# Kernel tuning notes

Hardware: AMD Instinct MI355X
Metric: run time of the kernel (lower is better)

Reference implementation:

```python
import jax, jax.numpy as jnp
import numpy as np

N = 50000      # nodes
E = 800000     # edges
D = 256        # embed_dim
H = 8          # num_heads
HD = D // H    # head_dim = 32
F = 4 * D      # feedforward_dim = 1024
SCALE = D ** -0.5  # note: module scales by embed_dim**-0.5, not head_dim
EPS = 1e-5


def setup_inputs() -> dict:
    key = jax.random.key(0)
    ks = jax.random.split(key, 10)
    x = jax.random.normal(ks[0], (N, D), dtype=jnp.float32)
    edge_indices = jax.random.randint(ks[1], (2, E), 0, N, dtype=jnp.int32)
    s = 0.02
    return {
        "x": x,
        "edge_indices": edge_indices,
        "w_qkv": jax.random.normal(ks[2], (D, 3 * D), dtype=jnp.float32) * s,
        "b_qkv": jnp.zeros((3 * D,), dtype=jnp.float32),
        "ln1_g": jnp.ones((D,), dtype=jnp.float32),
        "ln1_b": jnp.zeros((D,), dtype=jnp.float32),
        "ln2_g": jnp.ones((D,), dtype=jnp.float32),
        "ln2_b": jnp.zeros((D,), dtype=jnp.float32),
        "w1": jax.random.normal(ks[3], (D, F), dtype=jnp.float32) * s,
        "b1": jnp.zeros((F,), dtype=jnp.float32),
        "w2": jax.random.normal(ks[4], (F, D), dtype=jnp.float32) * s,
        "b2": jnp.zeros((D,), dtype=jnp.float32),
    }


def _layer_norm(x, g, b):
    m = jnp.mean(x, axis=-1, keepdims=True)
    v = jnp.mean((x - m) ** 2, axis=-1, keepdims=True)
    return (x - m) * jax.lax.rsqrt(v + EPS) * g + b


def _self_attention(x, edge_indices, w_qkv, b_qkv):
    qkv = (x @ w_qkv + b_qkv).reshape(N, H, 3 * HD)
    q, k, v = qkv[..., :HD], qkv[..., HD:2 * HD], qkv[..., 2 * HD:]
    rows, cols = edge_indices[0], edge_indices[1]
    # per-edge, per-head attention logits: [E, H]
    alpha = jnp.einsum('ehd,ehd->eh', q[rows], k[cols]) * SCALE
    # sparse softmax over each row (destination node) segment
    m = jax.ops.segment_max(alpha, rows, num_segments=N)       # [N, H]
    ea = jnp.exp(alpha - m[rows])                              # [E, H]
    denom = jax.ops.segment_sum(ea, rows, num_segments=N)      # [N, H]
    w = ea / denom[rows]                                       # [E, H]
    # per-head SpMM: out[r] += w_e * v[c]  -> [N, H, HD]
    out = jax.ops.segment_sum(w[:, :, None] * v[cols], rows, num_segments=N)
    return out.reshape(N, D)


def reference(x, edge_indices, w_qkv, b_qkv, ln1_g, ln1_b, ln2_g, ln2_b, w1, b1, w2, b2):
    # post-norm (norm_first=False), dropout=0
    x = _layer_norm(x + _self_attention(x, edge_indices, w_qkv, b_qkv), ln1_g, ln1_b)
    ffn = jax.nn.relu(x @ w1 + b1) @ w2 + b2
    x = _layer_norm(x + ffn, ln2_g, ln2_b)
    return x
```

## Files before the change

### kernel.cpp

```cpp
#include <hip/hip_runtime.h>
#include <hip/hip_bf16.h>

#define N_NODES 50000
#define E_EDGES 800000
#define D_MODEL 256
#define H_HEADS 8
#define HDIM    32
#define F_FFN   1024
#define ATT_SCALE 0.0625f
#define LN_EPS  1e-5f
#define NB_SCAN 196

typedef __attribute__((ext_vector_type(8))) short bf16x8;
typedef __attribute__((ext_vector_type(8))) unsigned short u16x8;
typedef __attribute__((ext_vector_type(4))) float f32x4;

__device__ __forceinline__ float bf2f(__hip_bfloat16 v) { return __bfloat162float(v); }
__device__ __forceinline__ __hip_bfloat16 f2bf(float v) { return __float2bfloat16(v); }
__device__ __forceinline__ unsigned short bfbits(float f) {
    __hip_bfloat16 h = __float2bfloat16(f);
    return *reinterpret_cast<unsigned short*>(&h);
}

__device__ __forceinline__ void unpack_bf8(uint4 u, float* f) {
    f[0] = __uint_as_float(u.x << 16); f[1] = __uint_as_float(u.x & 0xFFFF0000u);
    f[2] = __uint_as_float(u.y << 16); f[3] = __uint_as_float(u.y & 0xFFFF0000u);
    f[4] = __uint_as_float(u.z << 16); f[5] = __uint_as_float(u.z & 0xFFFF0000u);
    f[6] = __uint_as_float(u.w << 16); f[7] = __uint_as_float(u.w & 0xFFFF0000u);
}

template<int CTRL>
__device__ __forceinline__ float dpp_add(float v) {
    int t = __builtin_amdgcn_update_dpp(0, __float_as_int(v), CTRL, 0xF, 0xF, true);
    return v + __int_as_float(t);
}

__device__ __forceinline__ void load_lds16(const void* g, void* l) {
    __builtin_amdgcn_global_load_lds(
        (const __attribute__((address_space(1))) unsigned*)g,
        (__attribute__((address_space(3))) unsigned*)l, 16, 0, 0);
}

#define WAITV(N) asm volatile("s_waitcnt vmcnt(" #N ")" ::: "memory")
#define SBAR()   { __builtin_amdgcn_sched_barrier(0); __builtin_amdgcn_s_barrier(); \
                   __builtin_amdgcn_sched_barrier(0); }


#define PREP_X   3200000
#define PREP_WQ  (768 * 256)
#define PREP_W1  (1024 * 256)
#define PREP_W2  (256 * 1024)
#define PREP_BQ  768
#define PREP_B1  1024
#define PREP_TOT (PREP_X + PREP_WQ + PREP_W1 + PREP_W2 + PREP_BQ + PREP_B1 + N_NODES)
__global__ void prep_kernel(const float* __restrict__ x, unsigned short* __restrict__ xb,
                            const float* __restrict__ wq, __hip_bfloat16* __restrict__ wtq,
                            const float* __restrict__ w1, __hip_bfloat16* __restrict__ wt1,
                            const float* __restrict__ w2, __hip_bfloat16* __restrict__ wt2,
                            const float* __restrict__ bq, float* __restrict__ bqp,
                            const float* __restrict__ b1, float* __restrict__ b1p,
                            unsigned* __restrict__ counts, unsigned* __restrict__ cursor) {
    int i = blockIdx.x * blockDim.x + threadIdx.x;
    if (i < PREP_X) {
        float4 v = reinterpret_cast<const float4*>(x)[i];
        ushort4 o;
        o.x = bfbits(v.x); o.y = bfbits(v.y); o.z = bfbits(v.z); o.w = bfbits(v.w);
        reinterpret_cast<ushort4*>(xb)[i] = o;
        return;
    }
    i -= PREP_X;
    if (i < PREP_WQ) {
        int n = i >> 8, k = i & 255;
        int s = n >> 8, prel = n & 255;
        int d = (prel & 192) + ((prel & 15) << 2) + ((prel >> 4) & 3);
        int co = (d >> 5) * 96 + s * 32 + (d & 31);
        wtq[i] = f2bf(wq[(size_t)k * 768 + co]);
        return;
    }
    i -= PREP_WQ;
    if (i < PREP_W1) {
        int n = i >> 8, k = i & 255;
        int f = (n & ~63) + ((n & 15) << 2) + ((n >> 4) & 3);
        wt1[i] = f2bf(w1[(size_t)k * 1024 + f]);
        return;
    }
    i -= PREP_W1;
    if (i < PREP_W2) {
        int n = i >> 10, k = i & 1023;
        wt2[i] = f2bf(w2[(size_t)k * 256 + n]);
        return;
    }
    i -= PREP_W2;
    if (i < PREP_BQ) {
        int s = i >> 8, prel = i & 255;
        int d = (prel & 192) + ((prel & 15) << 2) + ((prel >> 4) & 3);
        bqp[i] = bq[(d >> 5) * 96 + s * 32 + (d & 31)];
        return;
    }
    i -= PREP_BQ;
    if (i < PREP_B1) {
        int f = (i & ~63) + ((i & 15) << 2) + ((i >> 4) & 3);
        b1p[i] = b1[f];
        return;
    }
    i -= PREP_B1;
    if (i < N_NODES) { counts[i] = 0u; cursor[i] = 0u; }
}

template<bool RELU, int EPI, int KT>
__global__ __launch_bounds__(256)
void mfma_gemm(const __hip_bfloat16* __restrict__ A,
               const __hip_bfloat16* __restrict__ Wt,
               const float* __restrict__ bias,
               __hip_bfloat16* __restrict__ outp,
               __hip_bfloat16* __restrict__ qb,
               unsigned char* __restrict__ kv8,
               int M, int Ncols) {
    __shared__ short Al[3][128 * 32];
    __shared__ short Bl[3][128 * 32];
    const int t = threadIdx.x;
    const int wave = t >> 6, lane = t & 63;

    unsigned flat = blockIdx.y * gridDim.x + blockIdx.x;
    unsigned nwg = gridDim.x * gridDim.y;
    unsigned q8 = nwg >> 3, r8 = nwg & 7;
    unsigned xcd = flat & 7, pos = flat >> 3;
    unsigned wg = (xcd < r8) ? (xcd * (q8 + 1) + pos)
                             : (r8 * (q8 + 1) + (xcd - r8) * q8 + pos);
    const int m0 = (int)(wg / gridDim.x) * 128;
    const int n0 = (int)(wg % gridDim.x) * 128;

    const int wr = wave >> 1, wc = wave & 1;

    const int srow = lane >> 2;
    const int skp  = (lane & 3) ^ ((lane >> 3) & 3);
    const int c0 = wave * 2;
    int ar0 = m0 + c0 * 16 + srow;      if (ar0 >= M) ar0 = M - 1;
    int ar1 = m0 + c0 * 16 + 16 + srow; if (ar1 >= M) ar1 = M - 1;
    const __hip_bfloat16* ga0 = A + (size_t)ar0 * KT + skp * 8;
    const __hip_bfloat16* ga1 = A + (size_t)ar1 * KT + skp * 8;
    const __hip_bfloat16* gb0 = Wt + (size_t)(n0 + c0 * 16 + srow) * KT + skp * 8;
    const __hip_bfloat16* gb1 = Wt + (size_t)(n0 + c0 * 16 + 16 + srow) * KT + skp * 8;

    const int lh = lane & 15, q = lane >> 4;
    const int qs = q ^ ((lane >> 1) & 3);
    const short* faB = &Al[0][(wr * 64 + lh) * 32 + qs * 8];
    const short* fbB = &Bl[0][(wc * 64 + lh) * 32 + qs * 8];

    f32x4 acc[4][4] = {};

#define GSTAGE(B)                                    \
    load_lds16(ga0, &Al[B][c0 * 512]);               \
    load_lds16(ga1, &Al[B][c0 * 512 + 512]);         \
    load_lds16(gb0, &Bl[B][c0 * 512]);               \
    load_lds16(gb1, &Bl[B][c0 * 512 + 512]);         \
    ga0 += 32; ga1 += 32; gb0 += 32; gb1 += 32;

#define GSTEP(FA, FB)                                                       \
    {                                                                       \
        bf16x8 af[4], bfr[4];                                               \
        _Pragma("unroll")                                                   \
        for (int i = 0; i < 4; i++) {                                       \
            af[i]  = *reinterpret_cast<const bf16x8*>((FA) + i * 16 * 32);  \
            bfr[i] = *reinterpret_cast<const bf16x8*>((FB) + i * 16 * 32);  \
        }                                                                   \
        _Pragma("unroll")                                                   \
        for (int mi = 0; mi < 4; mi++)                                      \
            _Pragma("unroll")                                               \
            for (int nj = 0; nj < 4; nj++)                                  \
                acc[mi][nj] = __builtin_amdgcn_mfma_f32_16x16x32_bf16(      \
                    af[mi], bfr[nj], acc[mi][nj], 0, 0, 0);                 \
    }

    constexpr int ns = KT >> 5;
    GSTAGE(0)
    GSTAGE(1)
#pragma unroll
    for (int s = 0; s < ns; ++s) {
        if (s < ns - 1) { WAITV(4); } else { WAITV(0); }
        SBAR();
        if (s + 2 < ns) {
            switch ((s + 2) % 3) {
                case 0: { GSTAGE(0) } break;
                case 1: { GSTAGE(1) } break;
                default: { GSTAGE(2) } break;
            }
        }
        const short* fa = faB + (s % 3) * 4096;
        const short* fb = fbB + (s % 3) * 4096;
        GSTEP(fa, fb)
    }
#undef GSTAGE
#undef GSTEP

    const int B = n0 + wc * 64;
    const int gnbase = B + lh;
    float bv[4];
#pragma unroll
    for (int nj = 0; nj < 4; nj++) bv[nj] = bias[gnbase + nj * 16];

    if (EPI == 0) {
        const int sec = B >> 8;
        const int c = ((B & 255) >> 6) * 16 + lh;
#pragma unroll
        for (int mi = 0; mi < 4; mi++) {
            int gmb = m0 + wr * 64 + mi * 16 + q * 4;
#pragma unroll
            for (int r = 0; r < 4; r++) {
                int gm = gmb + r;
                if (gm >= M) continue;
                float v0 = acc[mi][0][r] + bv[0];
                float v1 = acc[mi][1][r] + bv[1];
                float v2 = acc[mi][2][r] + bv[2];
                float v3 = acc[mi][3][r] + bv[3];
                if (sec == 0) {
                    ushort4 o;
                    o.x = bfbits(v0); o.y = bfbits(v1); o.z = bfbits(v2); o.w = bfbits(v3);
                    *reinterpret_cast<ushort4*>(qb + (size_t)gm * 256 + c * 4) = o;
                } else {
                    unsigned u = (unsigned)__builtin_amdgcn_cvt_pk_fp8_f32(v0, v1, 0, false);
                    u = (unsigned)__builtin_amdgcn_cvt_pk_fp8_f32(v2, v3, (int)u, true);
                    *reinterpret_cast<unsigned*>(
                        kv8 + (size_t)gm * 512 + c * 8 + (sec == 1 ? 0 : 4)) = u;
                }
            }
        }
    } else {
        const int cb = B + lh * 4;
#pragma unroll
        for (int mi = 0; mi < 4; mi++) {
            int gmb = m0 + wr * 64 + mi * 16 + q * 4;
#pragma unroll
            for (int r = 0; r < 4; r++) {
                int gm = gmb + r;
                if (gm >= M) continue;
                float v0 = acc[mi][0][r] + bv[0];
                float v1 = acc[mi][1][r] + bv[1];
                float v2 = acc[mi][2][r] + bv[2];
                float v3 = acc[mi][3][r] + bv[3];
                if (RELU) {
                    v0 = fmaxf(v0, 0.f); v1 = fmaxf(v1, 0.f);
                    v2 = fmaxf(v2, 0.f); v3 = fmaxf(v3, 0.f);
                }
                ushort4 o;
                o.x = bfbits(v0); o.y = bfbits(v1); o.z = bfbits(v2); o.w = bfbits(v3);
                *reinterpret_cast<ushort4*>(outp + (size_t)gm * Ncols + cb) = o;
            }
        }
    }
}

__global__ __launch_bounds__(512)
void ffn2_ln_kernel(const __hip_bfloat16* __restrict__ A,
                    const __hip_bfloat16* __restrict__ Wt,
                    const float* __restrict__ bias,
                    const __hip_bfloat16* __restrict__ resid,
                    const float* __restrict__ g, const float* __restrict__ bb,
                    float* __restrict__ out, int M) {
    __shared__ short LDS[3][(64 + 256) * 32];
    const int t = threadIdx.x;
    const int wave = t >> 6, lane = t & 63;
    const int m0 = blockIdx.x * 64;
    const int wr = wave >> 2, wc = wave & 3;

    const int srow = lane >> 2;
    const int skp  = (lane & 3) ^ ((lane >> 3) & 3);

    const __hip_bfloat16* gsrc0; int loff0;
    const __hip_bfloat16* gsrc1; int loff1;
    const __hip_bfloat16* gsrc2; int loff2;
    {
#define STAGE_INIT(GS, LO, C)                                            \
        if ((C) < 4) {                                                   \
            int r_ = m0 + (C) * 16 + srow; if (r_ >= M) r_ = M - 1;      \
            GS = A + (size_t)r_ * 1024 + skp * 8;                        \
            LO = (C) * 512;                                              \
        } else {                                                         \
            GS = Wt + (size_t)(((C) - 4) * 16 + srow) * 1024 + skp * 8;  \
            LO = 2048 + ((C) - 4) * 512;                                 \
        }
        STAGE_INIT(gsrc0, loff0, wave)
        STAGE_INIT(gsrc1, loff1, wave + 8)
        int c2 = (wave < 4) ? wave + 16 : 16;
        STAGE_INIT(gsrc2, loff2, c2)
#undef STAGE_INIT
    }

    const int lh = lane & 15, q = lane >> 4;
    const int qs = q ^ ((lane >> 1) & 3);
    const short* faB = &LDS[0][(wr * 32 + lh) * 32 + qs * 8];
    const short* fbB = &LDS[0][2048 + (wc * 64 + lh) * 32 + qs * 8];

    f32x4 acc[2][4] = {};

#define FFN2_STAGE(BUF)                                      \
    load_lds16(gsrc0, &LDS[BUF][loff0]);                     \
    load_lds16(gsrc1, &LDS[BUF][loff1]);                     \
    if (wave < 4) load_lds16(gsrc2, &LDS[BUF][loff2]);       \
    gsrc0 += 32; gsrc1 += 32; gsrc2 += 32;

#define FFN2_STEP(FA, FB)                                                   \
    {                                                                       \
        bf16x8 af[2], bfr[4];                                               \
        _Pragma("unroll")                                                   \
        for (int i = 0; i < 2; i++)                                         \
            af[i] = *reinterpret_cast<const bf16x8*>((FA) + i * 16 * 32);   \
        _Pragma("unroll")                                                   \
        for (int i = 0; i < 4; i++)                                         \
            bfr[i] = *reinterpret_cast<const bf16x8*>((FB) + i * 16 * 32);  \
        _Pragma("unroll")                                                   \
        for (int mi = 0; mi < 2; mi++)                                      \
            _Pragma("unroll")                                               \
            for (int nj = 0; nj < 4; nj++)                                  \
                acc[mi][nj] = __builtin_amdgcn_mfma_f32_16x16x32_bf16(      \
                    af[mi], bfr[nj], acc[mi][nj], 0, 0, 0);                 \
    }

    FFN2_STAGE(0)
    FFN2_STAGE(1)
#pragma unroll
    for (int s = 0; s < 32; ++s) {
        if (s < 31) {
            if (wave < 4) { WAITV(3); } else { WAITV(2); }
        } else {
            WAITV(0);
        }
        SBAR();
        if (s + 2 < 32) {
            switch ((s + 2) % 3) {
                case 0: { FFN2_STAGE(0) } break;
                case 1: { FFN2_STAGE(1) } break;
                default: { FFN2_STAGE(2) } break;
            }
        }
        const short* fa = faB + (s % 3) * 10240;
        const short* fb = fbB + (s % 3) * 10240;
        FFN2_STEP(fa, fb)
    }
    WAITV(0);
    SBAR();
#undef FFN2_STAGE
#undef FFN2_STEP

    const int colbase = wc * 64 + lh;
    float bv[4], gv[4], bbv[4];
#pragma unroll
    for (int nj = 0; nj < 4; nj++) {
        bv[nj]  = bias[colbase + nj * 16];
        gv[nj]  = g[colbase + nj * 16];
        bbv[nj] = bb[colbase + nj * 16];
    }

    float ps[2][4], pq[2][4];
#pragma unroll
    for (int mi = 0; mi < 2; mi++) {
#pragma unroll
        for (int r = 0; r < 4; r++) {
            int gm = m0 + wr * 32 + mi * 16 + q * 4 + r;
            int rgm = (gm < M) ? gm : M - 1;
            float s = 0.f, s2 = 0.f;
#pragma unroll
            for (int nj = 0; nj < 4; nj++) {
                float v = acc[mi][nj][r] + bv[nj]
                        + bf2f(resid[(size_t)rgm * 256 + colbase + nj * 16]);
                acc[mi][nj][r] = v;
                s += v; s2 += v * v;
            }
            ps[mi][r] = s; pq[mi][r] = s2;
        }
    }
#pragma unroll
    for (int off = 1; off <= 8; off <<= 1) {
#pragma unroll
        for (int mi = 0; mi < 2; mi++)
#pragma unroll
            for (int r = 0; r < 4; r++) {
                ps[mi][r] += __shfl_xor(ps[mi][r], off);
                pq[mi][r] += __shfl_xor(pq[mi][r], off);
            }
    }
    float* rs = (float*)(&LDS[0][0]);
    float* rq = rs + 256;
    if (lh == 0) {
#pragma unroll
        for (int mi = 0; mi < 2; mi++)
#pragma unroll
            for (int r = 0; r < 4; r++) {
                int m = wr * 32 + mi * 16 + q * 4 + r;
                rs[m * 4 + wc] = ps[mi][r];
                rq[m * 4 + wc] = pq[mi][r];
            }
    }
    __syncthreads();

#pragma unroll
    for (int mi = 0; mi < 2; mi++) {
#pragma unroll
        for (int r = 0; r < 4; r++) {
            int m = wr * 32 + mi * 16 + q * 4 + r;
            int gm = m0 + m;
            if (gm >= M) continue;
            float4 rsv = *reinterpret_cast<const float4*>(&rs[m * 4]);
            float4 rqv = *reinterpret_cast<const float4*>(&rq[m * 4]);
            float S  = (rsv.x + rsv.y) + (rsv.z + rsv.w);
            float S2 = (rqv.x + rqv.y) + (rqv.z + rqv.w);
            float mean = S * (1.f / (float)D_MODEL);
            float var  = S2 * (1.f / (float)D_MODEL) - mean * mean;
            float inv  = rsqrtf(var + LN_EPS);
#pragma unroll
            for (int nj = 0; nj < 4; nj++)
                out[(size_t)gm * 256 + colbase + nj * 16] =
                    (acc[mi][nj][r] - mean) * inv * gv[nj] + bbv[nj];
        }
    }
}

__global__ void count_kernel(const int* __restrict__ rows, unsigned* __restrict__ counts) {
    int e = blockIdx.x * blockDim.x + threadIdx.x;
    if (e < E_EDGES) atomicAdd(&counts[rows[e]], 1u);
}

__global__ void scan_blk_kernel(const unsigned* __restrict__ counts,
                                unsigned* __restrict__ offs, unsigned* __restrict__ bsum) {
    __shared__ unsigned sh[256];
    int t = threadIdx.x;
    int i = blockIdx.x * 256 + t;
    unsigned v = (i < N_NODES) ? counts[i] : 0u;
    sh[t] = v;
    __syncthreads();
#pragma unroll
    for (int off = 1; off < 256; off <<= 1) {
        unsigned u = (t >= off) ? sh[t - off] : 0u;
        __syncthreads();
        sh[t] += u;
        __syncthreads();
    }
    if (i < N_NODES) offs[i] = sh[t] - v;
    if (t == 255) bsum[blockIdx.x] = sh[255];
}

__global__ void scan_top_kernel(const unsigned* __restrict__ bsum, unsigned* __restrict__ bpre) {
    __shared__ unsigned sh[256];
    int t = threadIdx.x;
    unsigned v = (t < NB_SCAN) ? bsum[t] : 0u;
    sh[t] = v;
    __syncthreads();
#pragma unroll
    for (int off = 1; off < 256; off <<= 1) {
        unsigned u = (t >= off) ? sh[t - off] : 0u;
        __syncthreads();
        sh[t] += u;
        __syncthreads();
    }
    if (t < NB_SCAN) bpre[t] = sh[t] - v;
    if (t == NB_SCAN - 1) bpre[NB_SCAN] = sh[t];
}

__global__ void scatter_kernel(const int* __restrict__ rows, const int* __restrict__ cols,
                               const unsigned* __restrict__ offsets,
                               const unsigned* __restrict__ bpre,
                               unsigned* __restrict__ cursor,
                               int* __restrict__ scol) {
    int e = blockIdx.x * blockDim.x + threadIdx.x;
    if (e >= E_EDGES) return;
    int r = rows[e];
    unsigned idx = atomicAdd(&cursor[r], 1u);
    scol[offsets[r] + bpre[r >> 8] + idx] = cols[e];
}

__global__ __launch_bounds__(128)
void att_agg_kernel(const __hip_bfloat16* __restrict__ qb,
                    const unsigned char* __restrict__ kv8,
                    const unsigned* __restrict__ offsets,
                    const unsigned* __restrict__ bpre,
                    const int* __restrict__ scol,
                    const __hip_bfloat16* __restrict__ xres,
                    const float* __restrict__ g, const float* __restrict__ bb,
                    __hip_bfloat16* __restrict__ xn) {
    int n = blockIdx.x * 2 + (threadIdx.x >> 6);
    if (n >= N_NODES) return;
    const int lam = threadIdx.x & 63;
    const int hl  = lam & 31;
    const int sel = lam >> 5;
    const unsigned hlb = hl * 16;
    unsigned beg = offsets[n] + bpre[n >> 8];
    unsigned end = (n + 1 == N_NODES) ? bpre[NB_SCAN]
                                      : offsets[n + 1] + bpre[(n + 1) >> 8];

    float qv[8];
    {
        uint4 u = *reinterpret_cast<const uint4*>(qb + (size_t)n * 256 + hl * 8);
        unpack_bf8(u, qv);
#pragma unroll
        for (int i = 0; i < 8; i++) qv[i] *= ATT_SCALE;
    }

    float acc[8] = {};
    float l = 0.f;

#define PAIR_BODY(W, VMUL)                                                      \
    {                                                                           \
        auto k01 = __builtin_amdgcn_cvt_pk_f32_fp8((int)(W).x, false);          \
        auto k23 = __builtin_amdgcn_cvt_pk_f32_fp8((int)(W).x, true);           \
        auto k45 = __builtin_amdgcn_cvt_pk_f32_fp8((int)(W).z, false);          \
        auto k67 = __builtin_amdgcn_cvt_pk_f32_fp8((int)(W).z, true);           \
        float sv = qv[0] * k01[0] + qv[1] * k01[1] + qv[2] * k23[0]             \
                 + qv[3] * k23[1] + qv[4] * k45[0] + qv[5] * k45[1]             \
                 + qv[6] * k67[0] + qv[7] * k67[1];                             \
        sv = dpp_add<0xB1>(sv);                           \
        sv = dpp_add<0x4E>(sv);                           \
        float pv = __expf(sv) * (VMUL);                                         \
        l += pv;                                                                \
        auto v01 = __builtin_amdgcn_cvt_pk_f32_fp8((int)(W).y, false);          \
        auto v23 = __builtin_amdgcn_cvt_pk_f32_fp8((int)(W).y, true);           \
        auto v45 = __builtin_amdgcn_cvt_pk_f32_fp8((int)(W).w, false);          \
        auto v67 = __builtin_amdgcn_cvt_pk_f32_fp8((int)(W).w, true);           \
        acc[0] += pv * v01[0]; acc[1] += pv * v01[1];                           \
        acc[2] += pv * v23[0]; acc[3] += pv * v23[1];                           \
        acc[4] += pv * v45[0]; acc[5] += pv * v45[1];                           \
        acc[6] += pv * v67[0]; acc[7] += pv * v67[1];                           \
    }

    unsigned e = beg;
    unsigned oA = 0, oB = 0, oC = 0, oD = 0;
    if (e + 8 <= end) {
        oA = ((unsigned)scol[e + sel])     << 9;
        oB = ((unsigned)scol[e + 2 + sel]) << 9;
        oC = ((unsigned)scol[e + 4 + sel]) << 9;
        oD = ((unsigned)scol[e + 6 + sel]) << 9;
    }
    while (e + 8 <= end) {
        uint4 wa = *reinterpret_cast<const uint4*>(kv8 + (oA + hlb));
        uint4 wb = *reinterpret_cast<const uint4*>(kv8 + (oB + hlb));
        uint4 wc = *reinterpret_cast<const uint4*>(kv8 + (oC + hlb));
        uint4 wd = *reinterpret_cast<const uint4*>(kv8 + (oD + hlb));
        e += 8;
        if (e + 8 <= end) {
            oA = ((unsigned)scol[e + sel])     << 9;
            oB = ((unsigned)scol[e + 2 + sel]) << 9;
            oC = ((unsigned)scol[e + 4 + sel]) << 9;
            oD = ((unsigned)scol[e + 6 + sel]) << 9;
        }
        PAIR_BODY(wa, 1.0f)
        PAIR_BODY(wb, 1.0f)
        PAIR_BODY(wc, 1.0f)
        PAIR_BODY(wd, 1.0f)
    }
    for (; e + 2 <= end; e += 2) {
        unsigned o0 = ((unsigned)scol[e + sel]) << 9;
        uint4 wa = *reinterpret_cast<const uint4*>(kv8 + (o0 + hlb));
        PAIR_BODY(wa, 1.0f)
    }
    if (e < end) {
        unsigned o0 = ((unsigned)scol[e]) << 9;
        uint4 wa = *reinterpret_cast<const uint4*>(kv8 + (o0 + hlb));
        PAIR_BODY(wa, sel ? 0.0f : 1.0f)
    }
#undef PAIR_BODY

    l += __shfl_xor(l, 32);
#pragma unroll
    for (int i = 0; i < 8; i++) acc[i] += __shfl_xor(acc[i], 32);

    float inv_l = (l > 0.f) ? 1.f / l : 0.f;

    float tv[8];
    {
        float xv[8];
        uint4 u = *reinterpret_cast<const uint4*>(xres + (size_t)n * D_MODEL + hl * 8);
        unpack_bf8(u, xv);
#pragma unroll
        for (int i = 0; i < 8; i++) tv[i] = acc[i] * inv_l + xv[i];
    }

    float s = 0.f, s2 = 0.f;
#pragma unroll
    for (int i = 0; i < 8; i++) { s += tv[i]; s2 += tv[i] * tv[i]; }
#pragma unroll
    for (int off = 1; off <= 16; off <<= 1) {
        s  += __shfl_xor(s, off);
        s2 += __shfl_xor(s2, off);
    }
    float mean = s * (1.f / (float)D_MODEL);
    float var  = s2 * (1.f / (float)D_MODEL) - mean * mean;
    float inv  = rsqrtf(var + LN_EPS);

    if (sel == 0) {
        const float4* gp = reinterpret_cast<const float4*>(g);
        const float4* bp = reinterpret_cast<const float4*>(bb);
        float4 g0 = gp[hl * 2], g1 = gp[hl * 2 + 1];
        float4 b0 = bp[hl * 2], b1 = bp[hl * 2 + 1];
        float gv[8] = {g0.x, g0.y, g0.z, g0.w, g1.x, g1.y, g1.z, g1.w};
        float bv[8] = {b0.x, b0.y, b0.z, b0.w, b1.x, b1.y, b1.z, b1.w};
        u16x8 o;
#pragma unroll
        for (int i = 0; i < 8; i++)
            o[i] = bfbits((tv[i] - mean) * inv * gv[i] + bv[i]);
        *reinterpret_cast<u16x8*>(xn + (size_t)n * D_MODEL + hl * 8) = o;
    }
}

extern "C" void kernel_launch(void* const* d_in, const int* in_sizes, int n_in,
                              void* d_out, int out_size, void* d_ws, size_t ws_size,
                              hipStream_t stream) {
    const float* x     = (const float*)d_in[0];
    const int*   ei    = (const int*)d_in[1];
    const float* w_qkv = (const float*)d_in[2];
    const float* b_qkv = (const float*)d_in[3];
    const float* ln1_g = (const float*)d_in[4];
    const float* ln1_b = (const float*)d_in[5];
    const float* ln2_g = (const float*)d_in[6];
    const float* ln2_b = (const float*)d_in[7];
    const float* w1    = (const float*)d_in[8];
    const float* b1    = (const float*)d_in[9];
    const float* w2    = (const float*)d_in[10];
    const float* b2    = (const float*)d_in[11];
    const int* rows = ei;
    const int* cols = ei + E_EDGES;

    char* ws = (char*)d_ws;
    __hip_bfloat16* qb      = (__hip_bfloat16*)(ws + 0);
    unsigned char*  kv8     = (unsigned char*)(ws + 25600000);
    __hip_bfloat16* hbuf    = (__hip_bfloat16*)(ws + 0);
    __hip_bfloat16* xb      = (__hip_bfloat16*)(ws + 102400000);
    __hip_bfloat16* wtq     = (__hip_bfloat16*)(ws + 128000000);
    __hip_bfloat16* wt1     = (__hip_bfloat16*)(ws + 128400000);
    __hip_bfloat16* wt2     = (__hip_bfloat16*)(ws + 129000000);
    unsigned*       counts  = (unsigned*)(ws + 129600000);
    unsigned*       offsets = (unsigned*)(ws + 129800000);
    unsigned*       cursor  = (unsigned*)(ws + 130000008);
    int*            scol    = (int*)(ws + 130200008);
    unsigned*       bsum    = (unsigned*)(ws + 133400008);
    unsigned*       bpre    = (unsigned*)(ws + 133401032);
    float*          bqp     = (float*)(ws + 133500000);
    float*          b1p     = (float*)(ws + 133510000);
    __hip_bfloat16* xn      = (__hip_bfloat16*)(ws + 153600000);

    const int nbM = (N_NODES + 127) / 128;

    prep_kernel<<<(PREP_TOT + 255) / 256, 256, 0, stream>>>(
        x, (unsigned short*)xb, w_qkv, wtq, w1, wt1, w2, wt2,
        b_qkv, bqp, b1, b1p, counts, cursor);

    mfma_gemm<false, 0, 256><<<dim3(768 / 128, nbM), 256, 0, stream>>>(
        xb, wtq, bqp, nullptr, qb, kv8, N_NODES, 768);

    count_kernel<<<(E_EDGES + 255) / 256, 256, 0, stream>>>(rows, counts);
    scan_blk_kernel<<<NB_SCAN, 256, 0, stream>>>(counts, offsets, bsum);
    scan_top_kernel<<<1, 256, 0, stream>>>(bsum, bpre);
    scatter_kernel<<<(E_EDGES + 255) / 256, 256, 0, stream>>>(rows, cols, offsets, bpre,
                                                              cursor, scol);

    att_agg_kernel<<<(N_NODES + 1) / 2, 128, 0, stream>>>(qb, kv8, offsets, bpre, scol,
                                                          xb, ln1_g, ln1_b, xn);

    mfma_gemm<true, 1, 256><<<dim3(F_FFN / 128, nbM), 256, 0, stream>>>(
        xn, wt1, b1p, hbuf, nullptr, nullptr, N_NODES, F_FFN);

    ffn2_ln_kernel<<<(N_NODES + 63) / 64, 512, 0, stream>>>(hbuf, wt2, b2, xn, ln2_g, ln2_b,
                                                            (float*)d_out, N_NODES);
}
```

Measured before the change: 409.2 us.

## Fuse FFN1 GEMM, ReLU, FFN2 GEMM and LayerNorm into one kernel

Replaces the separate FFN1 GEMM (which wrote a 50000x1024 bf16 hidden buffer to global memory) and the FFN2+LN kernel with one fused kernel. Each 64-row block keeps its xn tile in LDS, computes the hidden activations in 256-wide chunks into LDS with a swizzled layout, and immediately accumulates them into the second GEMM. This removes the hidden-tensor round trip to HBM and one launch. In exchange, weight loads are now single-buffered and synchronous (no pipelining), with two barriers per k-step, and the weights are re-read by every block.

```diff
diff --git a/kernel.cpp b/kernel.cpp
--- a/kernel.cpp
+++ b/kernel.cpp
@@ -42,6 +42,7 @@
 }
 
 #define WAITV(N) asm volatile("s_waitcnt vmcnt(" #N ")" ::: "memory")
+#define WAITL()  asm volatile("s_waitcnt lgkmcnt(0)" ::: "memory")
 #define SBAR()   { __builtin_amdgcn_sched_barrier(0); __builtin_amdgcn_s_barrier(); \
                    __builtin_amdgcn_sched_barrier(0); }
 
@@ -107,15 +108,14 @@
     if (i < N_NODES) { counts[i] = 0u; cursor[i] = 0u; }
 }
 
-template<bool RELU, int EPI, int KT>
+template<int KT>
 __global__ __launch_bounds__(256)
 void mfma_gemm(const __hip_bfloat16* __restrict__ A,
                const __hip_bfloat16* __restrict__ Wt,
                const float* __restrict__ bias,
-               __hip_bfloat16* __restrict__ outp,
                __hip_bfloat16* __restrict__ qb,
                unsigned char* __restrict__ kv8,
-               int M, int Ncols) {
+               int M) {
     __shared__ short Al[3][128 * 32];
     __shared__ short Bl[3][128 * 32];
     const int t = threadIdx.x;
@@ -199,154 +199,149 @@
 #pragma unroll
     for (int nj = 0; nj < 4; nj++) bv[nj] = bias[gnbase + nj * 16];
 
-    if (EPI == 0) {
-        const int sec = B >> 8;
-        const int c = ((B & 255) >> 6) * 16 + lh;
-#pragma unroll
-        for (int mi = 0; mi < 4; mi++) {
-            int gmb = m0 + wr * 64 + mi * 16 + q * 4;
-#pragma unroll
-            for (int r = 0; r < 4; r++) {
-                int gm = gmb + r;
-                if (gm >= M) continue;
-                float v0 = acc[mi][0][r] + bv[0];
-                float v1 = acc[mi][1][r] + bv[1];
-                float v2 = acc[mi][2][r] + bv[2];
-                float v3 = acc[mi][3][r] + bv[3];
-                if (sec == 0) {
-                    ushort4 o;
-                    o.x = bfbits(v0); o.y = bfbits(v1); o.z = bfbits(v2); o.w = bfbits(v3);
-                    *reinterpret_cast<ushort4*>(qb + (size_t)gm * 256 + c * 4) = o;
-                } else {
-                    unsigned u = (unsigned)__builtin_amdgcn_cvt_pk_fp8_f32(v0, v1, 0, false);
-                    u = (unsigned)__builtin_amdgcn_cvt_pk_fp8_f32(v2, v3, (int)u, true);
-                    *reinterpret_cast<unsigned*>(
-                        kv8 + (size_t)gm * 512 + c * 8 + (sec == 1 ? 0 : 4)) = u;
-                }
-            }
-        }
-    } else {
-        const int cb = B + lh * 4;
-#pragma unroll
-        for (int mi = 0; mi < 4; mi++) {
-            int gmb = m0 + wr * 64 + mi * 16 + q * 4;
-#pragma unroll
-            for (int r = 0; r < 4; r++) {
-                int gm = gmb + r;
-                if (gm >= M) continue;
-                float v0 = acc[mi][0][r] + bv[0];
-                float v1 = acc[mi][1][r] + bv[1];
-                float v2 = acc[mi][2][r] + bv[2];
-                float v3 = acc[mi][3][r] + bv[3];
-                if (RELU) {
-                    v0 = fmaxf(v0, 0.f); v1 = fmaxf(v1, 0.f);
-                    v2 = fmaxf(v2, 0.f); v3 = fmaxf(v3, 0.f);
-                }
+    const int sec = B >> 8;
+    const int c = ((B & 255) >> 6) * 16 + lh;
+#pragma unroll
+    for (int mi = 0; mi < 4; mi++) {
+        int gmb = m0 + wr * 64 + mi * 16 + q * 4;
+#pragma unroll
+        for (int r = 0; r < 4; r++) {
+            int gm = gmb + r;
+            if (gm >= M) continue;
+            float v0 = acc[mi][0][r] + bv[0];
+            float v1 = acc[mi][1][r] + bv[1];
+            float v2 = acc[mi][2][r] + bv[2];
+            float v3 = acc[mi][3][r] + bv[3];
+            if (sec == 0) {
                 ushort4 o;
                 o.x = bfbits(v0); o.y = bfbits(v1); o.z = bfbits(v2); o.w = bfbits(v3);
-                *reinterpret_cast<ushort4*>(outp + (size_t)gm * Ncols + cb) = o;
+                *reinterpret_cast<ushort4*>(qb + (size_t)gm * 256 + c * 4) = o;
+            } else {
+                unsigned u = (unsigned)__builtin_amdgcn_cvt_pk_fp8_f32(v0, v1, 0, false);
+                u = (unsigned)__builtin_amdgcn_cvt_pk_fp8_f32(v2, v3, (int)u, true);
+                *reinterpret_cast<unsigned*>(
+                    kv8 + (size_t)gm * 512 + c * 8 + (sec == 1 ? 0 : 4)) = u;
             }
         }
     }
 }
 
-__global__ __launch_bounds__(512)
-void ffn2_ln_kernel(const __hip_bfloat16* __restrict__ A,
-                    const __hip_bfloat16* __restrict__ Wt,
-                    const float* __restrict__ bias,
-                    const __hip_bfloat16* __restrict__ resid,
-                    const float* __restrict__ g, const float* __restrict__ bb,
-                    float* __restrict__ out, int M) {
-    __shared__ short LDS[3][(64 + 256) * 32];
+__global__ __launch_bounds__(512, 4)
+void ffn_fused_kernel(const __hip_bfloat16* __restrict__ xn,
+                      const __hip_bfloat16* __restrict__ wt1p,
+                      const float* __restrict__ b1p,
+                      const __hip_bfloat16* __restrict__ wt2t,
+                      const float* __restrict__ b2,
+                      const float* __restrict__ g, const float* __restrict__ bb,
+                      float* __restrict__ out, int M) {
+    __shared__ short xnl[8 * 64 * 32];
+    __shared__ short hl[64 * 256];
+    __shared__ short Bl[256 * 32];
     const int t = threadIdx.x;
     const int wave = t >> 6, lane = t & 63;
     const int m0 = blockIdx.x * 64;
     const int wr = wave >> 2, wc = wave & 3;
-
     const int srow = lane >> 2;
     const int skp  = (lane & 3) ^ ((lane >> 3) & 3);
-
-    const __hip_bfloat16* gsrc0; int loff0;
-    const __hip_bfloat16* gsrc1; int loff1;
-    const __hip_bfloat16* gsrc2; int loff2;
-    {
-#define STAGE_INIT(GS, LO, C)                                            \
-        if ((C) < 4) {                                                   \
-            int r_ = m0 + (C) * 16 + srow; if (r_ >= M) r_ = M - 1;      \
-            GS = A + (size_t)r_ * 1024 + skp * 8;                        \
-            LO = (C) * 512;                                              \
-        } else {                                                         \
-            GS = Wt + (size_t)(((C) - 4) * 16 + srow) * 1024 + skp * 8;  \
-            LO = 2048 + ((C) - 4) * 512;                                 \
-        }
-        STAGE_INIT(gsrc0, loff0, wave)
-        STAGE_INIT(gsrc1, loff1, wave + 8)
-        int c2 = (wave < 4) ? wave + 16 : 16;
-        STAGE_INIT(gsrc2, loff2, c2)
-#undef STAGE_INIT
-    }
-
     const int lh = lane & 15, q = lane >> 4;
     const int qs = q ^ ((lane >> 1) & 3);
-    const short* faB = &LDS[0][(wr * 32 + lh) * 32 + qs * 8];
-    const short* fbB = &LDS[0][2048 + (wc * 64 + lh) * 32 + qs * 8];
-
-    f32x4 acc[2][4] = {};
-
-#define FFN2_STAGE(BUF)                                      \
-    load_lds16(gsrc0, &LDS[BUF][loff0]);                     \
-    load_lds16(gsrc1, &LDS[BUF][loff1]);                     \
-    if (wave < 4) load_lds16(gsrc2, &LDS[BUF][loff2]);       \
-    gsrc0 += 32; gsrc1 += 32; gsrc2 += 32;
-
-#define FFN2_STEP(FA, FB)                                                   \
-    {                                                                       \
-        bf16x8 af[2], bfr[4];                                               \
-        _Pragma("unroll")                                                   \
-        for (int i = 0; i < 2; i++)                                         \
-            af[i] = *reinterpret_cast<const bf16x8*>((FA) + i * 16 * 32);   \
-        _Pragma("unroll")                                                   \
-        for (int i = 0; i < 4; i++)                                         \
-            bfr[i] = *reinterpret_cast<const bf16x8*>((FB) + i * 16 * 32);  \
-        _Pragma("unroll")                                                   \
-        for (int mi = 0; mi < 2; mi++)                                      \
-            _Pragma("unroll")                                               \
-            for (int nj = 0; nj < 4; nj++)                                  \
-                acc[mi][nj] = __builtin_amdgcn_mfma_f32_16x16x32_bf16(      \
-                    af[mi], bfr[nj], acc[mi][nj], 0, 0, 0);                 \
-    }
-
-    FFN2_STAGE(0)
-    FFN2_STAGE(1)
-#pragma unroll
-    for (int s = 0; s < 32; ++s) {
-        if (s < 31) {
-            if (wave < 4) { WAITV(3); } else { WAITV(2); }
-        } else {
+    char* hb = (char*)hl;
+
+    for (int i = wave; i < 32; i += 8) {
+        int ks = i >> 2, c16 = i & 3;
+        int r_ = m0 + c16 * 16 + srow; if (r_ >= M) r_ = M - 1;
+        load_lds16(xn + (size_t)r_ * 256 + ks * 32 + skp * 8,
+                   &xnl[ks * 2048 + c16 * 512]);
+    }
+
+    f32x4 acc2[2][4] = {};
+
+    const int c16a = wave * 2, c16b = wave * 2 + 1;
+
+    for (int fc = 0; fc < 4; ++fc) {
+        f32x4 acc1[2][4] = {};
+        for (int s = 0; s < 8; ++s) {
+            SBAR();
+            load_lds16(wt1p + (size_t)(fc * 256 + c16a * 16 + srow) * 256 + s * 32 + skp * 8,
+                       &Bl[c16a * 512]);
+            load_lds16(wt1p + (size_t)(fc * 256 + c16b * 16 + srow) * 256 + s * 32 + skp * 8,
+                       &Bl[c16b * 512]);
             WAITV(0);
-        }
+            SBAR();
+            bf16x8 af[2], bfr[4];
+#pragma unroll
+            for (int mi = 0; mi < 2; mi++)
+                af[mi] = *reinterpret_cast<const bf16x8*>(
+                    &xnl[s * 2048 + (wr * 32 + mi * 16 + lh) * 32 + qs * 8]);
+#pragma unroll
+            for (int nj = 0; nj < 4; nj++)
+                bfr[nj] = *reinterpret_cast<const bf16x8*>(
+                    &Bl[(wc * 64 + nj * 16 + lh) * 32 + qs * 8]);
+#pragma unroll
+            for (int mi = 0; mi < 2; mi++)
+#pragma unroll
+                for (int nj = 0; nj < 4; nj++)
+                    acc1[mi][nj] = __builtin_amdgcn_mfma_f32_16x16x32_bf16(
+                        af[mi], bfr[nj], acc1[mi][nj], 0, 0, 0);
+        }
+        {
+            float bv1[4];
+#pragma unroll
+            for (int nj = 0; nj < 4; nj++)
+                bv1[nj] = b1p[fc * 256 + wc * 64 + lh + nj * 16];
+#pragma unroll
+            for (int mi = 0; mi < 2; mi++) {
+#pragma unroll
+                for (int r = 0; r < 4; r++) {
+                    int row = wr * 32 + mi * 16 + q * 4 + r;
+                    float v0 = fmaxf(acc1[mi][0][r] + bv1[0], 0.f);
+                    float v1 = fmaxf(acc1[mi][1][r] + bv1[1], 0.f);
+                    float v2 = fmaxf(acc1[mi][2][r] + bv1[2], 0.f);
+                    float v3 = fmaxf(acc1[mi][3][r] + bv1[3], 0.f);
+                    ushort4 o;
+                    o.x = bfbits(v0); o.y = bfbits(v1); o.z = bfbits(v2); o.w = bfbits(v3);
+                    unsigned off = (unsigned)(row * 512 + wc * 128 + lh * 8)
+                                 ^ (unsigned)((row & 7) << 4);
+                    *reinterpret_cast<ushort4*>(hb + off) = o;
+                }
+            }
+        }
+        WAITL();
         SBAR();
-        if (s + 2 < 32) {
-            switch ((s + 2) % 3) {
-                case 0: { FFN2_STAGE(0) } break;
-                case 1: { FFN2_STAGE(1) } break;
-                default: { FFN2_STAGE(2) } break;
+        for (int s = 0; s < 8; ++s) {
+            SBAR();
+            load_lds16(wt2t + (size_t)(c16a * 16 + srow) * 1024 + fc * 256 + s * 32 + skp * 8,
+                       &Bl[c16a * 512]);
+            load_lds16(wt2t + (size_t)(c16b * 16 + srow) * 1024 + fc * 256 + s * 32 + skp * 8,
+                       &Bl[c16b * 512]);
+            WAITV(0);
+            SBAR();
+            bf16x8 af[2], bfr[4];
+#pragma unroll
+            for (int mi = 0; mi < 2; mi++) {
+                int row = wr * 32 + mi * 16 + lh;
+                unsigned off = (unsigned)(row * 512 + s * 64 + q * 16)
+                             ^ (unsigned)((row & 7) << 4);
+                af[mi] = *reinterpret_cast<const bf16x8*>(hb + off);
             }
-        }
-        const short* fa = faB + (s % 3) * 10240;
-        const short* fb = fbB + (s % 3) * 10240;
-        FFN2_STEP(fa, fb)
-    }
-    WAITV(0);
-    SBAR();
-#undef FFN2_STAGE
-#undef FFN2_STEP
+#pragma unroll
+            for (int nj = 0; nj < 4; nj++)
+                bfr[nj] = *reinterpret_cast<const bf16x8*>(
+                    &Bl[(wc * 64 + nj * 16 + lh) * 32 + qs * 8]);
+#pragma unroll
+            for (int mi = 0; mi < 2; mi++)
+#pragma unroll
+                for (int nj = 0; nj < 4; nj++)
+                    acc2[mi][nj] = __builtin_amdgcn_mfma_f32_16x16x32_bf16(
+                        af[mi], bfr[nj], acc2[mi][nj], 0, 0, 0);
+        }
+    }
 
     const int colbase = wc * 64 + lh;
     float bv[4], gv[4], bbv[4];
 #pragma unroll
     for (int nj = 0; nj < 4; nj++) {
-        bv[nj]  = bias[colbase + nj * 16];
+        bv[nj]  = b2[colbase + nj * 16];
         gv[nj]  = g[colbase + nj * 16];
         bbv[nj] = bb[colbase + nj * 16];
     }
@@ -361,9 +356,9 @@
             float s = 0.f, s2 = 0.f;
 #pragma unroll
             for (int nj = 0; nj < 4; nj++) {
-                float v = acc[mi][nj][r] + bv[nj]
-                        + bf2f(resid[(size_t)rgm * 256 + colbase + nj * 16]);
-                acc[mi][nj][r] = v;
+                float v = acc2[mi][nj][r] + bv[nj]
+                        + bf2f(xn[(size_t)rgm * 256 + colbase + nj * 16]);
+                acc2[mi][nj][r] = v;
                 s += v; s2 += v * v;
             }
             ps[mi][r] = s; pq[mi][r] = s2;
@@ -379,8 +374,9 @@
                 pq[mi][r] += __shfl_xor(pq[mi][r], off);
             }
     }
-    float* rs = (float*)(&LDS[0][0]);
+    float* rs = (float*)(&xnl[0]);
     float* rq = rs + 256;
+    __syncthreads();
     if (lh == 0) {
 #pragma unroll
         for (int mi = 0; mi < 2; mi++)
@@ -410,7 +406,7 @@
 #pragma unroll
             for (int nj = 0; nj < 4; nj++)
                 out[(size_t)gm * 256 + colbase + nj * 16] =
-                    (acc[mi][nj][r] - mean) * inv * gv[nj] + bbv[nj];
+                    (acc2[mi][nj][r] - mean) * inv * gv[nj] + bbv[nj];
         }
     }
 }
@@ -507,8 +503,8 @@
         float sv = qv[0] * k01[0] + qv[1] * k01[1] + qv[2] * k23[0]             \
                  + qv[3] * k23[1] + qv[4] * k45[0] + qv[5] * k45[1]             \
                  + qv[6] * k67[0] + qv[7] * k67[1];                             \
-        sv = dpp_add<0xB1>(sv);                           \
-        sv = dpp_add<0x4E>(sv);                           \
+        sv = dpp_add<0xB1>(sv);                                                 \
+        sv = dpp_add<0x4E>(sv);                                                 \
         float pv = __expf(sv) * (VMUL);                                         \
         l += pv;                                                                \
         auto v01 = __builtin_amdgcn_cvt_pk_f32_fp8((int)(W).y, false);          \
@@ -621,7 +617,6 @@
     char* ws = (char*)d_ws;
     __hip_bfloat16* qb      = (__hip_bfloat16*)(ws + 0);
     unsigned char*  kv8     = (unsigned char*)(ws + 25600000);
-    __hip_bfloat16* hbuf    = (__hip_bfloat16*)(ws + 0);
     __hip_bfloat16* xb      = (__hip_bfloat16*)(ws + 102400000);
     __hip_bfloat16* wtq     = (__hip_bfloat16*)(ws + 128000000);
     __hip_bfloat16* wt1     = (__hip_bfloat16*)(ws + 128400000);
@@ -642,8 +637,8 @@
         x, (unsigned short*)xb, w_qkv, wtq, w1, wt1, w2, wt2,
         b_qkv, bqp, b1, b1p, counts, cursor);
 
-    mfma_gemm<false, 0, 256><<<dim3(768 / 128, nbM), 256, 0, stream>>>(
-        xb, wtq, bqp, nullptr, qb, kv8, N_NODES, 768);
+    mfma_gemm<256><<<dim3(768 / 128, nbM), 256, 0, stream>>>(
+        xb, wtq, bqp, qb, kv8, N_NODES);
 
     count_kernel<<<(E_EDGES + 255) / 256, 256, 0, stream>>>(rows, counts);
     scan_blk_kernel<<<NB_SCAN, 256, 0, stream>>>(counts, offsets, bsum);
@@ -654,9 +649,6 @@
     att_agg_kernel<<<(N_NODES + 1) / 2, 128, 0, stream>>>(qb, kv8, offsets, bpre, scol,
                                                           xb, ln1_g, ln1_b, xn);
 
-    mfma_gemm<true, 1, 256><<<dim3(F_FFN / 128, nbM), 256, 0, stream>>>(
-        xn, wt1, b1p, hbuf, nullptr, nullptr, N_NODES, F_FFN);
-
-    ffn2_ln_kernel<<<(N_NODES + 63) / 64, 512, 0, stream>>>(hbuf, wt2, b2, xn, ln2_g, ln2_b,
-                                                            (float*)d_out, N_NODES);
-}
+    ffn_fused_kernel<<<(N_NODES + 63) / 64, 512, 0, stream>>>(
+        xn, wt1, b1p, wt2, b2, ln2_g, ln2_b, (float*)d_out, N_NODES);
+}
```

New measurement: 414.9 us. About the same (+1.4%).
